# Performance work log

Measured on AMD Instinct MI355X. Metric: run time of the kernel, lower is better.

Reference implementation:

```python
import jax, jax.numpy as jnp
import numpy as np

N = 8192          # tokens
CD = 512          # coarse_dim
FD = 512          # fine_dim
CB = 4096         # coarse codebook size
FB = 8192         # fine codebook size
COST = 0.25       # commitment cost
LRELU = 0.1
EPS = 1e-5


def _vq(x, emb):
    # squared-distance cdist: [n, K]
    d = jnp.sum(x * x, axis=1, keepdims=True) + jnp.sum(emb * emb, axis=1) - 2.0 * (x @ emb.T)
    idx = jnp.argmin(d, axis=1)          # temperature=1.0 (updates=0); scaling doesn't change argmin
    q = emb[idx]                          # gather == one-hot @ emb, without materializing one-hot
    e_loss = jnp.mean((jax.lax.stop_gradient(q) - x) ** 2)
    q_loss = jnp.mean((q - jax.lax.stop_gradient(x)) ** 2)
    loss = q_loss + COST * e_loss
    q_st = x + jax.lax.stop_gradient(q - x)   # straight-through
    return q_st, loss


def _mlp(x, w, b, g, be):
    # Linear (torch: x @ W.T + b) -> LayerNorm -> LeakyReLU(0.1)
    h = x @ w.T + b
    m = jnp.mean(h, axis=-1, keepdims=True)
    v = jnp.var(h, axis=-1, keepdims=True)
    h = (h - m) / jnp.sqrt(v + EPS) * g + be
    return jnp.where(h > 0, h, LRELU * h)


def setup_inputs() -> dict:
    key = jax.random.key(0)
    ks = jax.random.split(key, 6)
    xav_c = float(np.sqrt(6.0 / (CB + CD)))
    xav_f = float(np.sqrt(6.0 / (FB + FD)))
    lin_s = float(np.sqrt(1.0 / CD))
    return {
        'z': jax.random.normal(ks[0], (N, CD + FD), dtype=jnp.float32),
        'coarse_emb': jax.random.uniform(ks[1], (CB, CD), jnp.float32, -xav_c, xav_c),
        'fine_emb': jax.random.uniform(ks[2], (FB, FD), jnp.float32, -xav_f, xav_f),
        'w_c2f': jax.random.uniform(ks[3], (FD, CD), jnp.float32, -lin_s, lin_s),
        'b_c2f': jnp.zeros((FD,), jnp.float32),
        'g_c2f': jnp.ones((FD,), jnp.float32),
        'be_c2f': jnp.zeros((FD,), jnp.float32),
        'w_f2c': jax.random.uniform(ks[4], (CD, FD), jnp.float32, -lin_s, lin_s),
        'b_f2c': jnp.zeros((CD,), jnp.float32),
        'g_f2c': jnp.ones((CD,), jnp.float32),
        'be_f2c': jnp.zeros((CD,), jnp.float32),
        'gate_c_raw': jnp.float32(0.5),
        'gate_f_raw': jnp.float32(0.5),
    }


def reference(z, coarse_emb, fine_emb, w_c2f, b_c2f, g_c2f, be_c2f,
              w_f2c, b_f2c, g_f2c, be_f2c, gate_c_raw, gate_f_raw):
    split = z.shape[1] // 2
    z_coarse, z_fine = z[:, :split], z[:, split:]

    z_coarse_q, coarse_loss = _vq(z_coarse, coarse_emb)
    coarse_influence = _mlp(jax.lax.stop_gradient(z_coarse_q), w_c2f, b_c2f, g_c2f, be_c2f)
    gate_c = jax.nn.sigmoid(gate_c_raw)

    residual = z_fine - gate_c * coarse_influence
    z_fine_q, fine_loss = _vq(residual, fine_emb)

    fine_feedback = _mlp(jax.lax.stop_gradient(z_fine_q), w_f2c, b_f2c, g_f2c, be_f2c)
    gate_f = jax.nn.sigmoid(gate_f_raw)

    z_coarse_corrected = z_coarse_q + 0.1 * gate_f * fine_feedback
    z_fine_reconstructed = z_fine_q + gate_c * coarse_influence
    z_hierarchical = jnp.concatenate([z_coarse_corrected, z_fine_reconstructed], axis=1)
    vq_loss = coarse_loss + fine_loss
    return z_hierarchical, vq_loss
```

## Files before the change

kernel.cpp:

```cpp
#include <hip/hip_runtime.h>
#include <hip/hip_bf16.h>
#include <cstdint>
#include <cstddef>

#define KD 512

#define OFF_CN   0u
#define OFF_FN   16384u
#define OFF_ZN   49152u
#define OFF_RN   81920u
#define OFF_LOSS 114688u
#define OFF_AMC  114944u
#define OFF_AMF  180480u
#define OFF_CEH  246016u
#define OFF_CEL  4440320u
#define OFF_FEH  8634624u
#define OFF_FEL  17023232u
#define OFF_ZCH  25411840u
#define OFF_ZCL  33800448u
#define OFF_RH   42189056u
#define OFF_RL   50577664u
#define OFF_W1H  58966272u
#define OFF_W1L  59490560u
#define OFF_W2H  60014848u
#define OFF_W2L  60539136u
#define OFF_H    61063424u
#define OFF_INFL 77840640u


typedef __attribute__((ext_vector_type(8))) short bf16x8;
typedef __attribute__((ext_vector_type(4))) float f32x4;
typedef unsigned long long u64;

__device__ __forceinline__ bf16x8 as_bf16x8(int4 v) {
  union { int4 i; bf16x8 b; } u; u.i = v; return u.b;
}

__device__ __forceinline__ float block_sum(float v, float* sred) {
#pragma unroll
  for (int off = 32; off > 0; off >>= 1) v += __shfl_down(v, off, 64);
  if ((threadIdx.x & 63) == 0) sred[threadIdx.x >> 6] = v;
  __syncthreads();
  float r = sred[0] + sred[1] + sred[2] + sred[3];
  __syncthreads();
  return r;
}

__device__ __forceinline__ float sigmoidf_(float x) { return 1.0f / (1.0f + expf(-x)); }

__device__ __forceinline__ void split_bf16(float v, __hip_bfloat16* hi, __hip_bfloat16* lo) {
  __hip_bfloat16 h = __float2bfloat16(v);
  *hi = h;
  *lo = __float2bfloat16(v - __bfloat162float(h));
}

__device__ __forceinline__ unsigned enc_sortable(float f) {
  unsigned u = __float_as_uint(f);
  return (u & 0x80000000u) ? ~u : (u | 0x80000000u);
}
__device__ __forceinline__ float dec_sortable(unsigned ub) {
  unsigned o = (ub & 0x80000000u) ? (ub & 0x7fffffffu) : ~ub;
  return __uint_as_float(o);
}
__device__ __forceinline__ u64 umin64(u64 a, u64 b) { return a < b ? a : b; }
__device__ __forceinline__ u64 umax64(u64 a, u64 b) { return a > b ? a : b; }

__device__ __forceinline__ void merge3(u64& a1, u64& a2, u64& a3, u64 b1, u64 b2, u64 b3) {
  u64 p = umax64(a1, b1);
  u64 q = umin64(a2, b2);
  u64 r = umax64(a2, b2);
  u64 s = umin64(a3, b3);
  u64 m1 = umin64(a1, b1);
  u64 m2 = umin64(p, q);
  u64 m3 = umin64(umin64(umax64(p, q), r), s);
  a1 = m1; a2 = m2; a3 = m3;
}

__global__ __launch_bounds__(256) void prep(
    const float* __restrict__ ce, const float* __restrict__ fe, const float* __restrict__ z,
    const float* __restrict__ w1, const float* __restrict__ w2,
    float* __restrict__ cn, float* __restrict__ fn, float* __restrict__ zn,
    __hip_bfloat16* __restrict__ ceH, __hip_bfloat16* __restrict__ ceL,
    __hip_bfloat16* __restrict__ feH, __hip_bfloat16* __restrict__ feL,
    __hip_bfloat16* __restrict__ zcF,
    __hip_bfloat16* __restrict__ w1H, __hip_bfloat16* __restrict__ w1L,
    __hip_bfloat16* __restrict__ w2H, __hip_bfloat16* __restrict__ w2L,
    float* __restrict__ lossp) {
  __shared__ float sred[4];
  const int b = blockIdx.x, t = threadIdx.x;
  const float* src;
  float* nd = nullptr;
  __hip_bfloat16 *dh = nullptr, *dl = nullptr;
  int fragMode = 0, hiOnly = 0;
  size_t row;
  if (b < 4096) {
    row = b; src = ce + row * KD; nd = cn + row; dh = ceH; dl = ceL; fragMode = 1;
  } else if (b < 12288) {
    row = b - 4096; src = fe + row * KD; nd = fn + row; dh = feH; dl = feL; fragMode = 1;
  } else if (b < 20480) {
    row = b - 12288; src = z + row * 1024; nd = zn + row; dh = zcF; fragMode = 1; hiOnly = 1;
  } else if (b < 20992) {
    row = b - 20480; src = w1 + row * KD; dh = w1H; dl = w1L;
  } else {
    row = b - 20992; src = w2 + row * KD; dh = w2H; dl = w2L;
  }
  float acc = 0.0f;
  if (fragMode) {
    float v0 = src[t], v1 = src[t + 256];
    if (hiOnly) {
      acc = v0 * v0;
      acc += v1 * v1;
    } else {
      acc = v0 * v0 + v1 * v1;
    }
  } else {
#pragma unroll
    for (int j = 0; j < 2; ++j) {
      int c = t + j * 256;
      float v = src[c];
      acc += v * v;
      __hip_bfloat16 h, l;
      split_bf16(v, &h, &l);
      dh[row * KD + c] = h;
      dl[row * KD + c] = l;
    }
  }
  if (nd) {
    float s = block_sum(acc, sred);
    if (t == 0) nd[0] = s;
  } else {
    __syncthreads();
    __syncthreads();
  }
  if (fragMode && t < 64) {
    union { int4 i; __hip_bfloat16 s[8]; } ph, pl;
#pragma unroll
    for (int j = 0; j < 8; ++j) {
      float v = src[8 * t + j];
      split_bf16(v, &ph.s[j], &pl.s[j]);
    }
    const int chunkIdx = (int)(((row >> 4) * 16 + (t >> 2)) * 64 +
                               ((size_t)((t & 3) << 4) | (row & 15)));
    ((int4*)dh)[chunkIdx] = ph.i;
    if (!hiOnly) ((int4*)dl)[chunkIdx] = pl.i;
  }
  if (b == 20480 && t == 0) lossp[0] = 0.0f;
}

__global__ __launch_bounds__(256, 2) void vq11(
    const int4* __restrict__ AfH,
    const int4* __restrict__ BfH,
    const float* __restrict__ cn,
    u64* __restrict__ bkeys) {
  __shared__ u64 sk[1536];
  const int t = threadIdx.x;
  const int w = t >> 6, l = t & 63;
  const int bx = blockIdx.x, by = blockIdx.y;
  const int rowTile = by << 8;
  const int colTile = bx << 7;
  const int NB = gridDim.y;

  const int rtg = rowTile >> 4;
  const int ctg = colTile >> 4;
  int aB[4], bB[8];
#pragma unroll
  for (int mt = 0; mt < 4; ++mt) aB[mt] = ((rtg + (w << 2) + mt) << 10) + l;
#pragma unroll
  for (int nt = 0; nt < 8; ++nt) bB[nt] = ((ctg + nt) << 10) + l;

  const int fr = l & 15;
  const int q = l >> 4;

  f32x4 acc[4][8];
#pragma unroll
  for (int i = 0; i < 4; ++i)
#pragma unroll
    for (int j = 0; j < 8; ++j) acc[i][j] = (f32x4){0.f, 0.f, 0.f, 0.f};

  int4 a0[4], b0[8];
#pragma unroll
  for (int mt = 0; mt < 4; ++mt) a0[mt] = AfH[aB[mt]];
#pragma unroll
  for (int nt = 0; nt < 8; ++nt) b0[nt] = BfH[bB[nt]];

#pragma unroll
  for (int i = 0; i < 16; ++i) {
    int4 a1[4], b1[8];
    if (i + 1 < 16) {
#pragma unroll
      for (int mt = 0; mt < 4; ++mt) a1[mt] = AfH[aB[mt] + ((i + 1) << 6)];
#pragma unroll
      for (int nt = 0; nt < 8; ++nt) b1[nt] = BfH[bB[nt] + ((i + 1) << 6)];
    }
    __builtin_amdgcn_s_setprio(1);
#pragma unroll
    for (int mt = 0; mt < 4; ++mt) {
      const bf16x8 af = as_bf16x8(a0[mt]);
#pragma unroll
      for (int nt = 0; nt < 8; ++nt)
        acc[mt][nt] = __builtin_amdgcn_mfma_f32_16x16x32_bf16(af, as_bf16x8(b0[nt]), acc[mt][nt], 0, 0, 0);
    }
    __builtin_amdgcn_s_setprio(0);
    if (i + 1 < 16) {
#pragma unroll
      for (int mt = 0; mt < 4; ++mt) a0[mt] = a1[mt];
#pragma unroll
      for (int nt = 0; nt < 8; ++nt) b0[nt] = b1[nt];
    }
  }

  u64 tk1[8], tk2[8], tk3[8];
#pragma unroll
  for (int nt = 0; nt < 8; ++nt) {
    u64 t1 = ~0ULL, t2 = ~0ULL, t3 = ~0ULL;
#pragma unroll
    for (int mt = 0; mt < 4; ++mt) {
#pragma unroll
      for (int reg = 0; reg < 4; ++reg) {
        const int code = rowTile + (w << 6) + (mt << 4) + (q << 2) + reg;
        float d = cn[code] - 2.0f * acc[mt][nt][reg];
        u64 key = ((u64)enc_sortable(d) << 32) | (u64)(unsigned)code;
        if (key < t1) { t3 = t2; t2 = t1; t1 = key; }
        else if (key < t2) { t3 = t2; t2 = key; }
        else if (key < t3) { t3 = key; }
      }
    }
#pragma unroll
    for (int off = 16; off <= 32; off <<= 1) {
      u64 b1 = __shfl_xor(t1, off, 64);
      u64 b2 = __shfl_xor(t2, off, 64);
      u64 b3 = __shfl_xor(t3, off, 64);
      merge3(t1, t2, t3, b1, b2, b3);
    }
    tk1[nt] = t1; tk2[nt] = t2; tk3[nt] = t3;
  }

  __syncthreads();
  if (w > 0 && l < 16) {
#pragma unroll
    for (int nt = 0; nt < 8; ++nt) {
      const int o = (((w << 3) + nt) * 16 + fr) * 3;
      sk[o] = tk1[nt]; sk[o + 1] = tk2[nt]; sk[o + 2] = tk3[nt];
    }
  }
  __syncthreads();
  if (w == 0 && l < 16) {
#pragma unroll
    for (int nt = 0; nt < 8; ++nt) {
      u64 t1 = tk1[nt], t2 = tk2[nt], t3 = tk3[nt];
#pragma unroll
      for (int wv = 1; wv < 4; ++wv) {
        const int o = (((wv << 3) + nt) * 16 + fr) * 3;
        merge3(t1, t2, t3, sk[o], sk[o + 1], sk[o + 2]);
      }
      const int query = colTile + (nt << 4) + fr;
      const size_t bo = ((size_t)query * NB + by) * 3;
      bkeys[bo] = t1; bkeys[bo + 1] = t2; bkeys[bo + 2] = t3;
    }
  }
}

__global__ __launch_bounds__(256) void rescue(
    const u64* __restrict__ bkeys, int NB3,
    const float* __restrict__ Q, int qStride,
    const float* __restrict__ Cb,
    const float* __restrict__ qn, const float* __restrict__ cnorm,
    float dscale, u64* __restrict__ am) {
  const int wv = threadIdx.x >> 6, l = threadIdx.x & 63;
  const int qi = (blockIdx.x << 2) + wv;
  const u64* kq = bkeys + (size_t)qi * NB3;
  u64 kk[3];
#pragma unroll
  for (int j = 0; j < 3; ++j) {
    const int idx = l + (j << 6);
    kk[j] = (idx < NB3) ? kq[idx] : ~0ULL;
  }
  u64 kmin = umin64(kk[0], umin64(kk[1], kk[2]));
#pragma unroll
  for (int off = 32; off > 0; off >>= 1) kmin = umin64(kmin, __shfl_xor(kmin, off, 64));
  const float xnv = qn[qi];
  const float dmin = dec_sortable((unsigned)(kmin >> 32));
  const float thr = dmin + dscale * sqrtf(xnv) + 0.01f;
  const u64 thrKey = ((u64)enc_sortable(thr) << 32) | 0xffffffffULL;

  const float* qrow = Q + (size_t)qi * qStride;
  const float4 qa = *(const float4*)(qrow + (l << 3));
  const float4 qb = *(const float4*)(qrow + (l << 3) + 4);
  float bestD = 3.4e38f;
  int bestC = 0x7fffffff;
#pragma unroll
  for (int j = 0; j < 3; ++j) {
    bool pend = kk[j] <= thrKey;
    u64 mask;
    while ((mask = __ballot(pend)) != 0ULL) {
      const int src = __ffsll((unsigned long long)mask) - 1;
      const u64 key = __shfl(kk[j], src, 64);
      if (l == src) pend = false;
      const int code = (int)(unsigned)(key & 0xffffffffULL);
      const float* crow = Cb + (size_t)code * KD;
      const float4 ca = *(const float4*)(crow + (l << 3));
      const float4 cb = *(const float4*)(crow + (l << 3) + 4);
      float dt = qa.x * ca.x + qa.y * ca.y + qa.z * ca.z + qa.w * ca.w +
                 qb.x * cb.x + qb.y * cb.y + qb.z * cb.z + qb.w * cb.w;
#pragma unroll
      for (int off = 32; off > 0; off >>= 1) dt += __shfl_xor(dt, off, 64);
      const float d = (xnv + cnorm[code]) - 2.0f * dt;
      if (d < bestD || (d == bestD && code < bestC)) { bestD = d; bestC = code; }
    }
  }
  if (l == 0) am[qi] = ((u64)enc_sortable(bestD) << 32) | (unsigned)bestC;
}

__global__ __launch_bounds__(256) void mlp6(
    const int4* __restrict__ AfH, const int4* __restrict__ AfL,
    const u64* __restrict__ gather,
    const __hip_bfloat16* __restrict__ Bh, const __hip_bfloat16* __restrict__ Bl,
    const float* __restrict__ bias, float* __restrict__ C) {
  __shared__ __align__(16) __hip_bfloat16 sAh[128 * 32];
  __shared__ __align__(16) __hip_bfloat16 sAl[128 * 32];
  __shared__ __align__(16) __hip_bfloat16 sBh[128 * 32];
  __shared__ __align__(16) __hip_bfloat16 sBl[128 * 32];
  const int t = threadIdx.x;
  const int w = t >> 6, l = t & 63;
  const int rowTile = blockIdx.y << 7;
  const int colTile = blockIdx.x << 7;
  const int wr = (w >> 1) << 6;
  const int wc = (w & 1) << 6;

  const int srow = t >> 2;
  const int sb = t & 3;
  const int skE = sb << 3;
  const int swz = (sb ^ ((srow >> 1) & 3)) << 3;
  const int wOff0 = (srow << 5) + swz;
  const int wOff1 = ((srow + 64) << 5) + swz;

  unsigned i0 = ((const unsigned*)gather)[2 * (rowTile + srow)];
  unsigned i1 = ((const unsigned*)gather)[2 * (rowTile + 64 + srow)];
  const int a0 = (int)((i0 >> 4) << 10) + (sb << 4) + (int)(i0 & 15);
  const int a1 = (int)((i1 >> 4) << 10) + (sb << 4) + (int)(i1 & 15);
  const size_t br0 = (size_t)(colTile + srow) * KD;
  const size_t br1 = (size_t)(colTile + 64 + srow) * KD;

  const int fr = l & 15;
  const int q = l >> 4;

  f32x4 acc[4][4];
#pragma unroll
  for (int i = 0; i < 4; ++i)
#pragma unroll
    for (int j = 0; j < 4; ++j) acc[i][j] = (f32x4){0.f, 0.f, 0.f, 0.f};

  for (int kk = 0; kk < KD; kk += 32) {
    const int kc64 = (kk >> 5) << 6;
    int4 vAh0 = AfH[a0 + kc64];
    int4 vAh1 = AfH[a1 + kc64];
    int4 vAl0 = AfL[a0 + kc64];
    int4 vAl1 = AfL[a1 + kc64];
    int4 vBh0 = *(const int4*)(Bh + br0 + kk + skE);
    int4 vBh1 = *(const int4*)(Bh + br1 + kk + skE);
    int4 vBl0 = *(const int4*)(Bl + br0 + kk + skE);
    int4 vBl1 = *(const int4*)(Bl + br1 + kk + skE);
    __syncthreads();
    *(int4*)(sAh + wOff0) = vAh0; *(int4*)(sAh + wOff1) = vAh1;
    *(int4*)(sAl + wOff0) = vAl0; *(int4*)(sAl + wOff1) = vAl1;
    *(int4*)(sBh + wOff0) = vBh0; *(int4*)(sBh + wOff1) = vBh1;
    *(int4*)(sBl + wOff0) = vBl0; *(int4*)(sBl + wOff1) = vBl1;
    __syncthreads();

    bf16x8 afh[4], afl[4], bfh[4], bfl[4];
#pragma unroll
    for (int mt = 0; mt < 4; ++mt) {
      const int rA = wr + (mt << 4) + fr;
      const int o = (rA << 5) + ((q ^ ((rA >> 1) & 3)) << 3);
      afh[mt] = *(const bf16x8*)(sAh + o);
      afl[mt] = *(const bf16x8*)(sAl + o);
    }
#pragma unroll
    for (int nt = 0; nt < 4; ++nt) {
      const int rB = wc + (nt << 4) + fr;
      const int o = (rB << 5) + ((q ^ ((rB >> 1) & 3)) << 3);
      bfh[nt] = *(const bf16x8*)(sBh + o);
      bfl[nt] = *(const bf16x8*)(sBl + o);
    }
#pragma unroll
    for (int mt = 0; mt < 4; ++mt)
#pragma unroll
      for (int nt = 0; nt < 4; ++nt) {
        acc[mt][nt] = __builtin_amdgcn_mfma_f32_16x16x32_bf16(afh[mt], bfh[nt], acc[mt][nt], 0, 0, 0);
        acc[mt][nt] = __builtin_amdgcn_mfma_f32_16x16x32_bf16(afh[mt], bfl[nt], acc[mt][nt], 0, 0, 0);
        acc[mt][nt] = __builtin_amdgcn_mfma_f32_16x16x32_bf16(afl[mt], bfh[nt], acc[mt][nt], 0, 0, 0);
      }
  }

  const int quad = l >> 4;
#pragma unroll
  for (int mt = 0; mt < 4; ++mt) {
#pragma unroll
    for (int reg = 0; reg < 4; ++reg) {
      const int row = rowTile + wr + (mt << 4) + (quad << 2) + reg;
#pragma unroll
      for (int nt = 0; nt < 4; ++nt) {
        const int col = colTile + wc + (nt << 4) + fr;
        C[(size_t)row * KD + col] = acc[mt][nt][reg] + bias[col];
      }
    }
  }
}

__global__ __launch_bounds__(256) void mlp1p(
    const int4* __restrict__ AfH,
    const u64* __restrict__ gather,
    const __hip_bfloat16* __restrict__ Bh,
    const float* __restrict__ bias, float* __restrict__ C) {
  __shared__ __align__(16) __hip_bfloat16 sAh[128 * 32];
  __shared__ __align__(16) __hip_bfloat16 sBh[128 * 32];
  const int t = threadIdx.x;
  const int w = t >> 6, l = t & 63;
  const int rowTile = blockIdx.y << 7;
  const int colTile = blockIdx.x << 7;
  const int wr = (w >> 1) << 6;
  const int wc = (w & 1) << 6;

  const int srow = t >> 2;
  const int sb = t & 3;
  const int skE = sb << 3;
  const int swz = (sb ^ ((srow >> 1) & 3)) << 3;
  const int wOff0 = (srow << 5) + swz;
  const int wOff1 = ((srow + 64) << 5) + swz;

  unsigned i0 = ((const unsigned*)gather)[2 * (rowTile + srow)];
  unsigned i1 = ((const unsigned*)gather)[2 * (rowTile + 64 + srow)];
  const int a0 = (int)((i0 >> 4) << 10) + (sb << 4) + (int)(i0 & 15);
  const int a1 = (int)((i1 >> 4) << 10) + (sb << 4) + (int)(i1 & 15);
  const size_t br0 = (size_t)(colTile + srow) * KD;
  const size_t br1 = (size_t)(colTile + 64 + srow) * KD;

  const int fr = l & 15;
  const int q = l >> 4;

  f32x4 acc[4][4];
#pragma unroll
  for (int i = 0; i < 4; ++i)
#pragma unroll
    for (int j = 0; j < 4; ++j) acc[i][j] = (f32x4){0.f, 0.f, 0.f, 0.f};

  for (int kk = 0; kk < KD; kk += 32) {
    const int kc64 = (kk >> 5) << 6;
    int4 vAh0 = AfH[a0 + kc64];
    int4 vAh1 = AfH[a1 + kc64];
    int4 vBh0 = *(const int4*)(Bh + br0 + kk + skE);
    int4 vBh1 = *(const int4*)(Bh + br1 + kk + skE);
    __syncthreads();
    *(int4*)(sAh + wOff0) = vAh0; *(int4*)(sAh + wOff1) = vAh1;
    *(int4*)(sBh + wOff0) = vBh0; *(int4*)(sBh + wOff1) = vBh1;
    __syncthreads();

    bf16x8 afh[4], bfh[4];
#pragma unroll
    for (int mt = 0; mt < 4; ++mt) {
      const int rA = wr + (mt << 4) + fr;
      const int o = (rA << 5) + ((q ^ ((rA >> 1) & 3)) << 3);
      afh[mt] = *(const bf16x8*)(sAh + o);
    }
#pragma unroll
    for (int nt = 0; nt < 4; ++nt) {
      const int rB = wc + (nt << 4) + fr;
      const int o = (rB << 5) + ((q ^ ((rB >> 1) & 3)) << 3);
      bfh[nt] = *(const bf16x8*)(sBh + o);
    }
#pragma unroll
    for (int mt = 0; mt < 4; ++mt)
#pragma unroll
      for (int nt = 0; nt < 4; ++nt)
        acc[mt][nt] = __builtin_amdgcn_mfma_f32_16x16x32_bf16(afh[mt], bfh[nt], acc[mt][nt], 0, 0, 0);
  }

  const int quad = l >> 4;
#pragma unroll
  for (int mt = 0; mt < 4; ++mt) {
#pragma unroll
    for (int reg = 0; reg < 4; ++reg) {
      const int row = rowTile + wr + (mt << 4) + (quad << 2) + reg;
#pragma unroll
      for (int nt = 0; nt < 4; ++nt) {
        const int col = colTile + wc + (nt << 4) + fr;
        C[(size_t)row * KD + col] = acc[mt][nt][reg] + bias[col];
      }
    }
  }
}

__global__ __launch_bounds__(256) void ln_residual(
    const float* __restrict__ h, const float* __restrict__ g, const float* __restrict__ be,
    const float* __restrict__ z, const float* __restrict__ gRaw,
    __hip_bfloat16* __restrict__ infl, float* __restrict__ rn,
    __hip_bfloat16* __restrict__ rF, float* __restrict__ resF) {
  __shared__ float sred[4];
  __shared__ float sr[512];
  const int row = blockIdx.x, t = threadIdx.x;
  const size_t base = (size_t)row * KD;
  float h0 = h[base + t], h1 = h[base + t + 256];
  float m = block_sum(h0 + h1, sred) * (1.0f / 512.0f);
  float d0 = h0 - m, d1 = h1 - m;
  float var = block_sum(d0 * d0 + d1 * d1, sred) * (1.0f / 512.0f);
  float sq = sqrtf(var + 1e-5f);
  float gc = sigmoidf_(gRaw[0]);
  float v0 = d0 / sq * g[t] + be[t];
  float v1 = d1 / sq * g[t + 256] + be[t + 256];
  v0 = v0 > 0.0f ? v0 : 0.1f * v0;
  v1 = v1 > 0.0f ? v1 : 0.1f * v1;
  infl[base + t] = __float2bfloat16(v0);
  infl[base + t + 256] = __float2bfloat16(v1);
  float zf0 = z[(size_t)row * 1024 + 512 + t];
  float zf1 = z[(size_t)row * 1024 + 512 + t + 256];
  float r0 = zf0 - gc * v0, r1 = zf1 - gc * v1;
  sr[t] = r0; sr[t + 256] = r1;
  resF[base + t] = r0;
  resF[base + t + 256] = r1;
  float rs = block_sum(r0 * r0 + r1 * r1, sred);
  if (t == 0) rn[row] = rs;
  if (t < 64) {
    union { int4 i; __hip_bfloat16 s[8]; } ph;
#pragma unroll
    for (int j = 0; j < 8; ++j) ph.s[j] = __float2bfloat16(sr[8 * t + j]);
    const int chunkIdx = (int)(((row >> 4) * 16 + (t >> 2)) * 64 +
                               ((size_t)((t & 3) << 4) | (row & 15)));
    ((int4*)rF)[chunkIdx] = ph.i;
  }
}

__global__ __launch_bounds__(256) void finalize(
    const float* __restrict__ h, const float* __restrict__ g, const float* __restrict__ be,
    const __hip_bfloat16* __restrict__ infl,
    const u64* __restrict__ amc, const u64* __restrict__ amf,
    const float* __restrict__ z, const float* __restrict__ ce, const float* __restrict__ fe,
    const float* __restrict__ gcRaw, const float* __restrict__ gfRaw,
    float* __restrict__ out, float* __restrict__ lossp) {
  __shared__ float sred[4];
  const int row = blockIdx.x, t = threadIdx.x;
  const size_t base = (size_t)row * KD;
  float h0 = h[base + t], h1 = h[base + t + 256];
  float m = block_sum(h0 + h1, sred) * (1.0f / 512.0f);
  float d0 = h0 - m, d1 = h1 - m;
  float var = block_sum(d0 * d0 + d1 * d1, sred) * (1.0f / 512.0f);
  float sq = sqrtf(var + 1e-5f);
  float fb0 = d0 / sq * g[t] + be[t];
  float fb1 = d1 / sq * g[t + 256] + be[t + 256];
  fb0 = fb0 > 0.0f ? fb0 : 0.1f * fb0;
  fb1 = fb1 > 0.0f ? fb1 : 0.1f * fb1;
  float gc = sigmoidf_(gcRaw[0]);
  float gf = sigmoidf_(gfRaw[0]);
  unsigned ic = (unsigned)(amc[row] & 0xffffffffULL);
  unsigned ifx = (unsigned)(amf[row] & 0xffffffffULL);
  float loc = 0.0f;
#pragma unroll
  for (int j = 0; j < 2; ++j) {
    int c = t + j * 256;
    float fb = j ? fb1 : fb0;
    float qc = ce[(size_t)ic * KD + c];
    float qf = fe[(size_t)ifx * KD + c];
    float zc = z[(size_t)row * 1024 + c];
    float zf = z[(size_t)row * 1024 + 512 + c];
    float fl = __bfloat162float(infl[base + c]);
    out[(size_t)row * 1024 + c] = qc + 0.1f * gf * fb;
    out[(size_t)row * 1024 + 512 + c] = qf + gc * fl;
    float dc = qc - zc;
    float res = zf - gc * fl;
    float df = qf - res;
    loc += dc * dc + df * df;
  }
  float ls = block_sum(loc, sred);
  if (t == 0) atomicAdd(lossp, ls);
}

__global__ void loss_write(const float* __restrict__ lossp, float* __restrict__ out) {
  out[0] = 1.25f * lossp[0] / (8192.0f * 512.0f);
}

extern "C" void kernel_launch(void* const* d_in, const int* in_sizes, int n_in,
                              void* d_out, int out_size, void* d_ws, size_t ws_size,
                              hipStream_t stream) {
  const float* z      = (const float*)d_in[0];
  const float* ce     = (const float*)d_in[1];
  const float* fe     = (const float*)d_in[2];
  const float* w_c2f  = (const float*)d_in[3];
  const float* b_c2f  = (const float*)d_in[4];
  const float* g_c2f  = (const float*)d_in[5];
  const float* be_c2f = (const float*)d_in[6];
  const float* w_f2c  = (const float*)d_in[7];
  const float* b_f2c  = (const float*)d_in[8];
  const float* g_f2c  = (const float*)d_in[9];
  const float* be_f2c = (const float*)d_in[10];
  const float* gcRaw  = (const float*)d_in[11];
  const float* gfRaw  = (const float*)d_in[12];
  float* out = (float*)d_out;
  char* ws = (char*)d_ws;

  float* cn = (float*)(ws + OFF_CN);
  float* fn = (float*)(ws + OFF_FN);
  float* zn = (float*)(ws + OFF_ZN);
  float* rn = (float*)(ws + OFF_RN);
  float* lossp = (float*)(ws + OFF_LOSS);
  u64* amc = (u64*)(ws + OFF_AMC);
  u64* amf = (u64*)(ws + OFF_AMF);
  __hip_bfloat16* ceH = (__hip_bfloat16*)(ws + OFF_CEH);
  __hip_bfloat16* ceL = (__hip_bfloat16*)(ws + OFF_CEL);
  __hip_bfloat16* feH = (__hip_bfloat16*)(ws + OFF_FEH);
  __hip_bfloat16* feL = (__hip_bfloat16*)(ws + OFF_FEL);
  __hip_bfloat16* zcF = (__hip_bfloat16*)(ws + OFF_ZCH);
  __hip_bfloat16* rF  = (__hip_bfloat16*)(ws + OFF_RH);
  __hip_bfloat16* w1H = (__hip_bfloat16*)(ws + OFF_W1H);
  __hip_bfloat16* w1L = (__hip_bfloat16*)(ws + OFF_W1L);
  __hip_bfloat16* w2H = (__hip_bfloat16*)(ws + OFF_W2H);
  __hip_bfloat16* w2L = (__hip_bfloat16*)(ws + OFF_W2L);
  float* h = (float*)(ws + OFF_H);
  __hip_bfloat16* infl = (__hip_bfloat16*)(ws + OFF_INFL);
  u64* bkeys = (u64*)(ws + OFF_H);
  float* resF = (float*)(ws + OFF_ZCH);

  prep<<<21504, 256, 0, stream>>>(ce, fe, z, w_c2f, w_f2c, cn, fn, zn,
                                  ceH, ceL, feH, feL, zcF,
                                  w1H, w1L, w2H, w2L, lossp);

  vq11<<<dim3(64, 16), 256, 0, stream>>>((const int4*)ceH, (const int4*)zcF, cn, bkeys);

  rescue<<<2048, 256, 0, stream>>>(bkeys, 48, z, 1024, ce, zn, cn, 0.00321f, amc);

  mlp6<<<dim3(4, 64), 256, 0, stream>>>((const int4*)ceH, (const int4*)ceL, amc,
                                        w1H, w1L, b_c2f, h);

  ln_residual<<<8192, 256, 0, stream>>>(h, g_c2f, be_c2f, z, gcRaw, infl, rn, rF, resF);

  vq11<<<dim3(64, 32), 256, 0, stream>>>((const int4*)feH, (const int4*)rF, fn, bkeys);

  rescue<<<2048, 256, 0, stream>>>(bkeys, 96, resF, 512, fe, rn, fn, 0.00233f, amf);

  mlp1p<<<dim3(4, 64), 256, 0, stream>>>((const int4*)feH, amf, w2H, b_f2c, h);

  finalize<<<8192, 256, 0, stream>>>(h, g_f2c, be_f2c, infl, amc, amf, z, ce, fe,
                                     gcRaw, gfRaw, out, lossp);
  loss_write<<<1, 1, 0, stream>>>(lossp, out + (size_t)8192 * 1024);
}
```

Before: 627.4 us.

## Stage query tile in LDS and double block row tile in VQ distance kernel

The VQ distance GEMM kernel now uses 512-thread blocks covering 512 codebook rows. The 128-query B tile is loaded once into LDS through global_load_lds, so eight waves share it instead of each wave reloading B fragments from global memory. Block IDs are remapped so blocks with the same row tile land on the same XCD, which should help L2 reuse. Fewer row blocks means fewer per-block top-3 candidates for the rescue pass, at the cost of 128KB of LDS per block, lower occupancy, and a wider cross-wave merge.

```diff
diff --git a/kernel.cpp b/kernel.cpp
--- a/kernel.cpp
+++ b/kernel.cpp
@@ -34,6 +34,12 @@
 
 __device__ __forceinline__ bf16x8 as_bf16x8(int4 v) {
   union { int4 i; bf16x8 b; } u; u.i = v; return u.b;
+}
+
+__device__ __forceinline__ void gl_lds16(const void* g, void* l) {
+  __builtin_amdgcn_global_load_lds(
+      (const __attribute__((address_space(1))) void*)g,
+      (__attribute__((address_space(3))) void*)l, 16, 0, 0);
 }
 
 __device__ __forceinline__ float block_sum(float v, float* sred) {
@@ -147,26 +153,36 @@
   if (b == 20480 && t == 0) lossp[0] = 0.0f;
 }
 
-__global__ __launch_bounds__(256, 2) void vq11(
+__global__ __launch_bounds__(512) void vq12(
     const int4* __restrict__ AfH,
     const int4* __restrict__ BfH,
     const float* __restrict__ cn,
     u64* __restrict__ bkeys) {
-  __shared__ u64 sk[1536];
+  __shared__ __align__(16) int4 sB[8192];
   const int t = threadIdx.x;
   const int w = t >> 6, l = t & 63;
-  const int bx = blockIdx.x, by = blockIdx.y;
-  const int rowTile = by << 8;
+
+  const int id = (int)blockIdx.x;
+  const int xcd = id & 7;
+  const int j = id >> 3;
+  const int ypp = (int)(gridDim.x >> 9);
+  const int bx = j & 63;
+  const int by = xcd * ypp + (j >> 6);
+  const int rowTile = by << 9;
   const int colTile = bx << 7;
-  const int NB = gridDim.y;
-
-  const int rtg = rowTile >> 4;
-  const int ctg = colTile >> 4;
-  int aB[4], bB[8];
-#pragma unroll
-  for (int mt = 0; mt < 4; ++mt) aB[mt] = ((rtg + (w << 2) + mt) << 10) + l;
-#pragma unroll
-  for (int nt = 0; nt < 8; ++nt) bB[nt] = ((ctg + nt) << 10) + l;
+  const int NB = (int)(gridDim.x >> 6);
+
+  const int4* bsrc = BfH + ((size_t)(colTile >> 4) << 10);
+#pragma unroll
+  for (int k = 0; k < 16; ++k)
+    gl_lds16(bsrc + (k << 9) + t, &sB[(k << 9) + t]);
+  asm volatile("s_waitcnt vmcnt(0)" ::: "memory");
+  __syncthreads();
+
+  const int rtg = (rowTile >> 4) + (w << 2);
+  int aB[4];
+#pragma unroll
+  for (int mt = 0; mt < 4; ++mt) aB[mt] = ((rtg + mt) << 10) + l;
 
   const int fr = l & 15;
   const int q = l >> 4;
@@ -175,37 +191,33 @@
 #pragma unroll
   for (int i = 0; i < 4; ++i)
 #pragma unroll
-    for (int j = 0; j < 8; ++j) acc[i][j] = (f32x4){0.f, 0.f, 0.f, 0.f};
-
-  int4 a0[4], b0[8];
+    for (int jj = 0; jj < 8; ++jj) acc[i][jj] = (f32x4){0.f, 0.f, 0.f, 0.f};
+
+  int4 a0[4], a1[4];
 #pragma unroll
   for (int mt = 0; mt < 4; ++mt) a0[mt] = AfH[aB[mt]];
-#pragma unroll
-  for (int nt = 0; nt < 8; ++nt) b0[nt] = BfH[bB[nt]];
 
 #pragma unroll
   for (int i = 0; i < 16; ++i) {
-    int4 a1[4], b1[8];
     if (i + 1 < 16) {
 #pragma unroll
       for (int mt = 0; mt < 4; ++mt) a1[mt] = AfH[aB[mt] + ((i + 1) << 6)];
-#pragma unroll
-      for (int nt = 0; nt < 8; ++nt) b1[nt] = BfH[bB[nt] + ((i + 1) << 6)];
-    }
+    }
+    bf16x8 af[4];
+#pragma unroll
+    for (int mt = 0; mt < 4; ++mt) af[mt] = as_bf16x8(a0[mt]);
     __builtin_amdgcn_s_setprio(1);
 #pragma unroll
-    for (int mt = 0; mt < 4; ++mt) {
-      const bf16x8 af = as_bf16x8(a0[mt]);
-#pragma unroll
-      for (int nt = 0; nt < 8; ++nt)
-        acc[mt][nt] = __builtin_amdgcn_mfma_f32_16x16x32_bf16(af, as_bf16x8(b0[nt]), acc[mt][nt], 0, 0, 0);
+    for (int nt = 0; nt < 8; ++nt) {
+      const bf16x8 bf = as_bf16x8(sB[(nt << 10) + (i << 6) + l]);
+#pragma unroll
+      for (int mt = 0; mt < 4; ++mt)
+        acc[mt][nt] = __builtin_amdgcn_mfma_f32_16x16x32_bf16(af[mt], bf, acc[mt][nt], 0, 0, 0);
     }
     __builtin_amdgcn_s_setprio(0);
     if (i + 1 < 16) {
 #pragma unroll
       for (int mt = 0; mt < 4; ++mt) a0[mt] = a1[mt];
-#pragma unroll
-      for (int nt = 0; nt < 8; ++nt) b0[nt] = b1[nt];
     }
   }
 
@@ -236,6 +248,7 @@
   }
 
   __syncthreads();
+  u64* sk = (u64*)sB;
   if (w > 0 && l < 16) {
 #pragma unroll
     for (int nt = 0; nt < 8; ++nt) {
@@ -249,7 +262,7 @@
     for (int nt = 0; nt < 8; ++nt) {
       u64 t1 = tk1[nt], t2 = tk2[nt], t3 = tk3[nt];
 #pragma unroll
-      for (int wv = 1; wv < 4; ++wv) {
+      for (int wv = 1; wv < 8; ++wv) {
         const int o = (((wv << 3) + nt) * 16 + fr) * 3;
         merge3(t1, t2, t3, sk[o], sk[o + 1], sk[o + 2]);
       }
@@ -622,18 +635,18 @@
                                   ceH, ceL, feH, feL, zcF,
                                   w1H, w1L, w2H, w2L, lossp);
 
-  vq11<<<dim3(64, 16), 256, 0, stream>>>((const int4*)ceH, (const int4*)zcF, cn, bkeys);
-
-  rescue<<<2048, 256, 0, stream>>>(bkeys, 48, z, 1024, ce, zn, cn, 0.00321f, amc);
+  vq12<<<512, 512, 0, stream>>>((const int4*)ceH, (const int4*)zcF, cn, bkeys);
+
+  rescue<<<2048, 256, 0, stream>>>(bkeys, 24, z, 1024, ce, zn, cn, 0.00321f, amc);
 
   mlp6<<<dim3(4, 64), 256, 0, stream>>>((const int4*)ceH, (const int4*)ceL, amc,
                                         w1H, w1L, b_c2f, h);
 
   ln_residual<<<8192, 256, 0, stream>>>(h, g_c2f, be_c2f, z, gcRaw, infl, rn, rF, resF);
 
-  vq11<<<dim3(64, 32), 256, 0, stream>>>((const int4*)feH, (const int4*)rF, fn, bkeys);
-
-  rescue<<<2048, 256, 0, stream>>>(bkeys, 96, resF, 512, fe, rn, fn, 0.00233f, amf);
+  vq12<<<1024, 512, 0, stream>>>((const int4*)feH, (const int4*)rF, fn, bkeys);
+
+  rescue<<<2048, 256, 0, stream>>>(bkeys, 48, resF, 512, fe, rn, fn, 0.00233f, amf);
 
   mlp1p<<<dim3(4, 64), 256, 0, stream>>>((const int4*)feH, amf, w2H, b_f2c, h);
 
```

Result: faster. 554.5 us (-11.6%).
